# Kernel tuning notes

Measured on AMD Instinct MI355X. Metric: run time of the kernel, lower is better.

The kernel has to match this reference:

```python
import jax, jax.numpy as jnp
from jax import lax
import numpy as np

B, N, C = 16, 4096, 64
NPOINT, NSAMPLE, RADIUS = 1024, 32, 0.2


def farthest_point_sample(xyz, npoint):
    # xyz: (B, N, 3) -> (B, npoint) int32 indices
    b, n, _ = xyz.shape

    def body(carry, _):
        dists, farthest = carry  # (B,N), (B,)
        centroid = jnp.take_along_axis(xyz, farthest[:, None, None], axis=1)  # (B,1,3)
        d = jnp.sum((xyz - centroid) ** 2, axis=-1)  # (B,N)
        dists = jnp.minimum(dists, d)
        nxt = jnp.argmax(dists, axis=-1).astype(jnp.int32)
        return (dists, nxt), farthest

    init = (jnp.full((b, n), 1e10, xyz.dtype), jnp.zeros((b,), jnp.int32))
    _, idx = lax.scan(body, init, None, length=npoint)
    return idx.T  # (B, npoint)


def ball_query(radius, nsample, xyz, new_xyz):
    # xyz: (B,N,3), new_xyz: (B,S,3) -> (B,S,nsample) int32
    n = xyz.shape[1]
    # squared distances via ||a||^2 - 2ab + ||b||^2 to avoid (B,S,N,3) temp
    sqr = (jnp.sum(new_xyz ** 2, -1)[:, :, None]
           - 2.0 * jnp.einsum('bsc,bnc->bsn', new_xyz, xyz)
           + jnp.sum(xyz ** 2, -1)[:, None, :])  # (B,S,N)
    cand = jnp.broadcast_to(jnp.arange(n, dtype=jnp.int32), sqr.shape)
    cand = jnp.where(sqr > radius * radius, n, cand)  # out-of-ball -> sentinel N
    idx = jnp.sort(cand, axis=-1)[..., :nsample]  # first nsample in-ball indices
    first = idx[..., :1]
    return jnp.where(idx == n, first, idx)  # pad with first neighbor


def gather_points(pts, idx):
    # pts: (B,N,C), idx: (B,S,K) -> (B,S,K,C)
    return jax.vmap(lambda p, i: p[i])(pts, idx)


def setup_inputs() -> dict:
    key = jax.random.key(0)
    ks = jax.random.split(key, 8)
    c_in = C + 3  # use_xyz=True
    mlp = [64, 64, 128]
    inp = {
        'xyz': jax.random.uniform(ks[0], (B, N, 3), dtype=jnp.float32),
        'points': jax.random.normal(ks[1], (B, N, C), dtype=jnp.float32),
    }
    dims = [c_in] + mlp
    for i in range(3):
        fan_in = dims[i]
        inp[f'w{i}'] = jax.random.normal(ks[2 + i], (dims[i], dims[i + 1]), dtype=jnp.float32) / np.sqrt(fan_in)
        inp[f'b{i}'] = jnp.zeros((dims[i + 1],), dtype=jnp.float32)
    return inp


def reference(xyz, points, w0, b0, w1, b1, w2, b2):
    fps_idx = farthest_point_sample(xyz, NPOINT)  # (B,S)
    new_xyz = jnp.take_along_axis(xyz, fps_idx[:, :, None], axis=1)  # (B,S,3)
    idx = ball_query(RADIUS, NSAMPLE, xyz, new_xyz)  # (B,S,K)

    grouped_xyz = gather_points(xyz, idx) - new_xyz[:, :, None, :]  # (B,S,K,3) local coords
    grouped_pts = gather_points(points, idx)  # (B,S,K,C)
    new_points = jnp.concatenate([grouped_xyz, grouped_pts], axis=-1)  # (B,S,K,3+C)

    for w, b in ((w0, b0), (w1, b1), (w2, b2)):  # pointwise 1x1 Conv2d MLP, relu, no bn
        new_points = jax.nn.relu(jnp.einsum('bskc,cd->bskd', new_points, w) + b)

    new_points = jnp.max(new_points, axis=2)  # max-pool over nsample -> (B,S,128)
    return new_xyz, new_points
```

## Files before the change

### kernel.cpp

```cpp
#include <hip/hip_runtime.h>
#include <cstdint>

#define Bn 16
#define Nn 4096
#define Cn 64
#define NPOINT 1024
#define NSAMPLE 32

typedef float f32x2 __attribute__((ext_vector_type(2)));

__device__ __forceinline__ unsigned long long fps_wave_max(unsigned long long k) {
#define FPS_STEP(CTRL)                                                          \
  {                                                                             \
    unsigned int lo = (unsigned int)k, hi = (unsigned int)(k >> 32);            \
    unsigned int tlo =                                                          \
        (unsigned int)__builtin_amdgcn_update_dpp((int)lo, (int)lo, CTRL, 0xF, 0xF, false); \
    unsigned int thi =                                                          \
        (unsigned int)__builtin_amdgcn_update_dpp((int)hi, (int)hi, CTRL, 0xF, 0xF, false); \
    unsigned long long t = ((unsigned long long)thi << 32) | tlo;               \
    if (t > k) k = t;                                                           \
  }
  FPS_STEP(0x111)
  FPS_STEP(0x112)
  FPS_STEP(0x114)
  FPS_STEP(0x118)
  FPS_STEP(0x142)
  FPS_STEP(0x143)
#undef FPS_STEP
  return k;
}

__global__ __launch_bounds__(256) void fps_kernel(const float* __restrict__ xyz,
                                                  float* __restrict__ new_xyz) {
  const int b = blockIdx.x;
  const int t = threadIdx.x;
  const float* px = xyz + b * Nn * 3;

  __shared__ __align__(16) float4 sp[Nn];
  __shared__ __align__(16) float sc[NPOINT * 3];
  __shared__ __align__(16) unsigned long long rk[2][4];

  f32x2 X2[8], Y2[8], Z2[8], D2[8];
#pragma unroll
  for (int p = 0; p < 8; ++p) {
    int i0 = (2 * p) * 256 + t;
    int i1 = (2 * p + 1) * 256 + t;
    float x0 = px[i0 * 3 + 0], y0 = px[i0 * 3 + 1], z0 = px[i0 * 3 + 2];
    float x1 = px[i1 * 3 + 0], y1 = px[i1 * 3 + 1], z1 = px[i1 * 3 + 2];
    sp[i0] = make_float4(x0, y0, z0, 0.0f);
    sp[i1] = make_float4(x1, y1, z1, 0.0f);
    X2[p] = (f32x2){x0, x1};
    Y2[p] = (f32x2){y0, y1};
    Z2[p] = (f32x2){z0, z1};
    D2[p] = (f32x2){1e10f, 1e10f};
  }
  __syncthreads();

  int far = 0;

  for (int it = 0; it < NPOINT; ++it) {
    float4 c = sp[far];
    if (t == 0) {
      sc[it * 3 + 0] = c.x;
      sc[it * 3 + 1] = c.y;
      sc[it * 3 + 2] = c.z;
    }

    f32x2 cx2 = {c.x, c.x};
    f32x2 cy2 = {c.y, c.y};
    f32x2 cz2 = {c.z, c.z};

    float bd = -1.0f;
    int   bi = 0;
#pragma unroll
    for (int p = 0; p < 8; ++p) {
#pragma clang fp contract(off)
      f32x2 dx = X2[p] - cx2;
      f32x2 dy = Y2[p] - cy2;
      f32x2 dz = Z2[p] - cz2;
      f32x2 d2 = (dx * dx + dy * dy) + dz * dz;
      f32x2 nd = __builtin_elementwise_min(D2[p], d2);
      D2[p] = nd;
      float n0 = nd[0];
      if (n0 > bd) { bd = n0; bi = (2 * p) * 256 + t; }
      float n1 = nd[1];
      if (n1 > bd) { bd = n1; bi = (2 * p + 1) * 256 + t; }
    }

    unsigned long long k =
        ((unsigned long long)__float_as_uint(bd) << 32) |
        (unsigned int)(~(unsigned int)bi);
    k = fps_wave_max(k);

    const int buf = it & 1;
    if ((t & 63) == 63) rk[buf][t >> 6] = k;
    __syncthreads();

    unsigned long long f0 = rk[buf][0];
    unsigned long long f1 = rk[buf][1];
    unsigned long long f2 = rk[buf][2];
    unsigned long long f3 = rk[buf][3];
    if (f1 > f0) f0 = f1;
    if (f2 > f0) f0 = f2;
    if (f3 > f0) f0 = f3;
    far = (int)(~(unsigned int)f0);
  }

  float* out = new_xyz + b * NPOINT * 3;
  for (int i = t; i < NPOINT * 3; i += 256) out[i] = sc[i];
}

__global__ __launch_bounds__(256) void ballquery_kernel(const float* __restrict__ xyz,
                                                        const float* __restrict__ new_xyz,
                                                        int* __restrict__ bidx) {
  const int gw = (int)((blockIdx.x * 256 + threadIdx.x) >> 6);
  const int lane = threadIdx.x & 63;
  if (gw >= Bn * NPOINT) return;
  const int b = gw >> 10;
  const float* px = xyz + b * Nn * 3;
  const float R2 = 0.04f;

  float cx = new_xyz[gw * 3 + 0];
  float cy = new_xyz[gw * 3 + 1];
  float cz = new_xyz[gw * 3 + 2];
  float cs;
  {
#pragma clang fp contract(off)
    cs = (cx * cx + cy * cy) + cz * cz;
  }

  int* out = bidx + gw * NSAMPLE;
  int found = 0;
  int first = -1;

  for (int base = 0; base < Nn && found < NSAMPLE; base += 64) {
    int i = base + lane;
    float x = px[i * 3 + 0];
    float y = px[i * 3 + 1];
    float z = px[i * 3 + 2];
    float ps, sqr;
    float dot = fmaf(cx, x, 0.0f);
    dot = fmaf(cy, y, dot);
    dot = fmaf(cz, z, dot);
    {
#pragma clang fp contract(off)
      ps = (x * x + y * y) + z * z;
      sqr = (cs - 2.0f * dot) + ps;
    }
    bool pass = !(sqr > R2);
    unsigned long long m = __ballot(pass);
    if (first < 0 && m) first = base + (__ffsll(m) - 1);
    int rank = (int)__popcll(m & ((1ULL << lane) - 1ULL));
    int pos = found + rank;
    if (pass && pos < NSAMPLE) out[pos] = i;
    found += (int)__popcll(m);
  }

  int cnt = found < NSAMPLE ? found : NSAMPLE;
  for (int k = cnt + lane; k < NSAMPLE; k += 64) out[k] = first;
}

__global__ __launch_bounds__(64) void group_mlp_kernel(
    const float* __restrict__ xyz, const float* __restrict__ points,
    const float* __restrict__ w0, const float* __restrict__ b0,
    const float* __restrict__ w1, const float* __restrict__ b1,
    const float* __restrict__ w2, const float* __restrict__ b2,
    const float* __restrict__ new_xyz, const int* __restrict__ bidx,
    float* __restrict__ out_pts) {
  const int lane = threadIdx.x & 63;
  const int g = blockIdx.x;
  const int b = g >> 10;

  __shared__ __align__(16) float Xw[NSAMPLE][68];
  __shared__ __align__(16) float Hw[NSAMPLE][64];

  const int* bi = bidx + g * NSAMPLE;
  const float c0 = new_xyz[g * 3 + 0];
  const float c1 = new_xyz[g * 3 + 1];
  const float c2 = new_xyz[g * 3 + 2];

  for (int k = 0; k < NSAMPLE; ++k) {
    int id = bi[k];
    float v;
    if (lane < 3) {
      v = xyz[(b * Nn + id) * 3 + lane] - (lane == 0 ? c0 : (lane == 1 ? c1 : c2));
    } else {
      v = points[(b * Nn + id) * Cn + (lane - 3)];
    }
    Xw[k][lane] = v;
    if (lane < 3) Xw[k][64 + lane] = points[(b * Nn + id) * Cn + 61 + lane];
  }

  float acc[NSAMPLE];

  {
    float bb = b0[lane];
#pragma unroll
    for (int k = 0; k < NSAMPLE; ++k) acc[k] = bb;
    for (int c4 = 0; c4 < 16; ++c4) {
      float wa = w0[(c4 * 4 + 0) * 64 + lane];
      float wb = w0[(c4 * 4 + 1) * 64 + lane];
      float wc = w0[(c4 * 4 + 2) * 64 + lane];
      float wd = w0[(c4 * 4 + 3) * 64 + lane];
#pragma unroll
      for (int k = 0; k < NSAMPLE; ++k) {
        float4 xv = *(const float4*)&Xw[k][c4 * 4];
        acc[k] += xv.x * wa + xv.y * wb + xv.z * wc + xv.w * wd;
      }
    }
    float wt0 = w0[64 * 64 + lane];
    float wt1 = w0[65 * 64 + lane];
    float wt2 = w0[66 * 64 + lane];
#pragma unroll
    for (int k = 0; k < NSAMPLE; ++k)
      acc[k] += Xw[k][64] * wt0 + Xw[k][65] * wt1 + Xw[k][66] * wt2;
#pragma unroll
    for (int k = 0; k < NSAMPLE; ++k) Hw[k][lane] = fmaxf(acc[k], 0.0f);
  }

  {
    float bb = b1[lane];
#pragma unroll
    for (int k = 0; k < NSAMPLE; ++k) acc[k] = bb;
    for (int c4 = 0; c4 < 16; ++c4) {
      float wa = w1[(c4 * 4 + 0) * 64 + lane];
      float wb = w1[(c4 * 4 + 1) * 64 + lane];
      float wc = w1[(c4 * 4 + 2) * 64 + lane];
      float wd = w1[(c4 * 4 + 3) * 64 + lane];
#pragma unroll
      for (int k = 0; k < NSAMPLE; ++k) {
        float4 hv = *(const float4*)&Hw[k][c4 * 4];
        acc[k] += hv.x * wa + hv.y * wb + hv.z * wc + hv.w * wd;
      }
    }
#pragma unroll
    for (int k = 0; k < NSAMPLE; ++k) Xw[k][lane] = fmaxf(acc[k], 0.0f);
  }

  {
    float accB[NSAMPLE];
    float bbA = b2[lane];
    float bbB = b2[lane + 64];
#pragma unroll
    for (int k = 0; k < NSAMPLE; ++k) { acc[k] = bbA; accB[k] = bbB; }
    for (int c4 = 0; c4 < 16; ++c4) {
      float wa = w2[(c4 * 4 + 0) * 128 + lane];
      float wb = w2[(c4 * 4 + 1) * 128 + lane];
      float wc = w2[(c4 * 4 + 2) * 128 + lane];
      float wd = w2[(c4 * 4 + 3) * 128 + lane];
      float we = w2[(c4 * 4 + 0) * 128 + lane + 64];
      float wf = w2[(c4 * 4 + 1) * 128 + lane + 64];
      float wg = w2[(c4 * 4 + 2) * 128 + lane + 64];
      float wh = w2[(c4 * 4 + 3) * 128 + lane + 64];
#pragma unroll
      for (int k = 0; k < NSAMPLE; ++k) {
        float4 xv = *(const float4*)&Xw[k][c4 * 4];
        acc[k]  += xv.x * wa + xv.y * wb + xv.z * wc + xv.w * wd;
        accB[k] += xv.x * we + xv.y * wf + xv.z * wg + xv.w * wh;
      }
    }
    float mA = 0.0f, mB = 0.0f;
#pragma unroll
    for (int k = 0; k < NSAMPLE; ++k) {
      mA = fmaxf(mA, acc[k]);
      mB = fmaxf(mB, accB[k]);
    }
    float* outp = out_pts + g * 128;
    outp[lane] = mA;
    outp[lane + 64] = mB;
  }
}

extern "C" void kernel_launch(void* const* d_in, const int* in_sizes, int n_in,
                              void* d_out, int out_size, void* d_ws, size_t ws_size,
                              hipStream_t stream) {
  const float* xyz    = (const float*)d_in[0];
  const float* points = (const float*)d_in[1];
  const float* w0     = (const float*)d_in[2];
  const float* b0     = (const float*)d_in[3];
  const float* w1     = (const float*)d_in[4];
  const float* b1     = (const float*)d_in[5];
  const float* w2     = (const float*)d_in[6];
  const float* b2     = (const float*)d_in[7];

  float* new_xyz = (float*)d_out;
  float* new_pts = (float*)d_out + Bn * NPOINT * 3;
  int*   bidx    = (int*)d_ws;

  fps_kernel<<<Bn, 256, 0, stream>>>(xyz, new_xyz);
  ballquery_kernel<<<(Bn * NPOINT) / 4, 256, 0, stream>>>(xyz, new_xyz, bidx);
  group_mlp_kernel<<<Bn * NPOINT, 64, 0, stream>>>(xyz, points, w0, b0, w1, b1,
                                                   w2, b2, new_xyz, bidx, new_pts);
}
```

Baseline: 1.198 ms.

## Widen FPS block to 512 threads and remap MLP to one sample per lane

FPS now runs 512 threads per batch, so each thread holds half as many points and the per-iteration distance loop is shorter, at the cost of a wider cross-wave reduction. The grouped MLP kernel is restructured so that each lane owns one neighbor sample and keeps 64 output-channel accumulators in registers. Weights are read as uniform broadcast loads, and two groups are processed per 64-lane block. The max-pool becomes a shuffle-xor reduction across 32 lanes. This removes the per-sample LDS float4 reads, but it raises register pressure and adds 5 shuffle rounds over 64 values per pass.

```diff
diff --git a/kernel.cpp b/kernel.cpp
--- a/kernel.cpp
+++ b/kernel.cpp
@@ -6,6 +6,11 @@
 #define Cn 64
 #define NPOINT 1024
 #define NSAMPLE 32
+
+#define FPS_T 512
+#define FPS_W (FPS_T / 64)
+#define FPS_P (Nn / FPS_T)
+#define FPS_PAIRS (FPS_P / 2)
 
 typedef float f32x2 __attribute__((ext_vector_type(2)));
 
@@ -30,21 +35,21 @@
   return k;
 }
 
-__global__ __launch_bounds__(256) void fps_kernel(const float* __restrict__ xyz,
-                                                  float* __restrict__ new_xyz) {
+__global__ __launch_bounds__(FPS_T) void fps_kernel(const float* __restrict__ xyz,
+                                                    float* __restrict__ new_xyz) {
   const int b = blockIdx.x;
   const int t = threadIdx.x;
   const float* px = xyz + b * Nn * 3;
 
   __shared__ __align__(16) float4 sp[Nn];
   __shared__ __align__(16) float sc[NPOINT * 3];
-  __shared__ __align__(16) unsigned long long rk[2][4];
-
-  f32x2 X2[8], Y2[8], Z2[8], D2[8];
-#pragma unroll
-  for (int p = 0; p < 8; ++p) {
-    int i0 = (2 * p) * 256 + t;
-    int i1 = (2 * p + 1) * 256 + t;
+  __shared__ __align__(16) unsigned long long rk[2][FPS_W];
+
+  f32x2 X2[FPS_PAIRS], Y2[FPS_PAIRS], Z2[FPS_PAIRS], D2[FPS_PAIRS];
+#pragma unroll
+  for (int p = 0; p < FPS_PAIRS; ++p) {
+    int i0 = (2 * p) * FPS_T + t;
+    int i1 = (2 * p + 1) * FPS_T + t;
     float x0 = px[i0 * 3 + 0], y0 = px[i0 * 3 + 1], z0 = px[i0 * 3 + 2];
     float x1 = px[i1 * 3 + 0], y1 = px[i1 * 3 + 1], z1 = px[i1 * 3 + 2];
     sp[i0] = make_float4(x0, y0, z0, 0.0f);
@@ -73,7 +78,7 @@
     float bd = -1.0f;
     int   bi = 0;
 #pragma unroll
-    for (int p = 0; p < 8; ++p) {
+    for (int p = 0; p < FPS_PAIRS; ++p) {
 #pragma clang fp contract(off)
       f32x2 dx = X2[p] - cx2;
       f32x2 dy = Y2[p] - cy2;
@@ -82,9 +87,9 @@
       f32x2 nd = __builtin_elementwise_min(D2[p], d2);
       D2[p] = nd;
       float n0 = nd[0];
-      if (n0 > bd) { bd = n0; bi = (2 * p) * 256 + t; }
+      if (n0 > bd) { bd = n0; bi = (2 * p) * FPS_T + t; }
       float n1 = nd[1];
-      if (n1 > bd) { bd = n1; bi = (2 * p + 1) * 256 + t; }
+      if (n1 > bd) { bd = n1; bi = (2 * p + 1) * FPS_T + t; }
     }
 
     unsigned long long k =
@@ -97,17 +102,16 @@
     __syncthreads();
 
     unsigned long long f0 = rk[buf][0];
-    unsigned long long f1 = rk[buf][1];
-    unsigned long long f2 = rk[buf][2];
-    unsigned long long f3 = rk[buf][3];
-    if (f1 > f0) f0 = f1;
-    if (f2 > f0) f0 = f2;
-    if (f3 > f0) f0 = f3;
+#pragma unroll
+    for (int w = 1; w < FPS_W; ++w) {
+      unsigned long long fw = rk[buf][w];
+      if (fw > f0) f0 = fw;
+    }
     far = (int)(~(unsigned int)f0);
   }
 
   float* out = new_xyz + b * NPOINT * 3;
-  for (int i = t; i < NPOINT * 3; i += 256) out[i] = sc[i];
+  for (int i = t; i < NPOINT * 3; i += FPS_T) out[i] = sc[i];
 }
 
 __global__ __launch_bounds__(256) void ballquery_kernel(const float* __restrict__ xyz,
@@ -167,107 +171,86 @@
     const float* __restrict__ w2, const float* __restrict__ b2,
     const float* __restrict__ new_xyz, const int* __restrict__ bidx,
     float* __restrict__ out_pts) {
-  const int lane = threadIdx.x & 63;
-  const int g = blockIdx.x;
+  const int lane = threadIdx.x;
+  const int k = lane & 31;
+  const int g = blockIdx.x * 2 + (lane >> 5);
   const int b = g >> 10;
 
-  __shared__ __align__(16) float Xw[NSAMPLE][68];
-  __shared__ __align__(16) float Hw[NSAMPLE][64];
-
-  const int* bi = bidx + g * NSAMPLE;
-  const float c0 = new_xyz[g * 3 + 0];
-  const float c1 = new_xyz[g * 3 + 1];
-  const float c2 = new_xyz[g * 3 + 2];
-
-  for (int k = 0; k < NSAMPLE; ++k) {
-    int id = bi[k];
-    float v;
-    if (lane < 3) {
-      v = xyz[(b * Nn + id) * 3 + lane] - (lane == 0 ? c0 : (lane == 1 ? c1 : c2));
-    } else {
-      v = points[(b * Nn + id) * Cn + (lane - 3)];
-    }
-    Xw[k][lane] = v;
-    if (lane < 3) Xw[k][64 + lane] = points[(b * Nn + id) * Cn + 61 + lane];
-  }
-
-  float acc[NSAMPLE];
+  __shared__ float Xs[68][64];
+
+  const int id = bidx[g * NSAMPLE + k];
 
   {
-    float bb = b0[lane];
-#pragma unroll
-    for (int k = 0; k < NSAMPLE; ++k) acc[k] = bb;
-    for (int c4 = 0; c4 < 16; ++c4) {
-      float wa = w0[(c4 * 4 + 0) * 64 + lane];
-      float wb = w0[(c4 * 4 + 1) * 64 + lane];
-      float wc = w0[(c4 * 4 + 2) * 64 + lane];
-      float wd = w0[(c4 * 4 + 3) * 64 + lane];
-#pragma unroll
-      for (int k = 0; k < NSAMPLE; ++k) {
-        float4 xv = *(const float4*)&Xw[k][c4 * 4];
-        acc[k] += xv.x * wa + xv.y * wb + xv.z * wc + xv.w * wd;
-      }
-    }
-    float wt0 = w0[64 * 64 + lane];
-    float wt1 = w0[65 * 64 + lane];
-    float wt2 = w0[66 * 64 + lane];
-#pragma unroll
-    for (int k = 0; k < NSAMPLE; ++k)
-      acc[k] += Xw[k][64] * wt0 + Xw[k][65] * wt1 + Xw[k][66] * wt2;
-#pragma unroll
-    for (int k = 0; k < NSAMPLE; ++k) Hw[k][lane] = fmaxf(acc[k], 0.0f);
-  }
-
+    const float* p3 = xyz + (b * Nn + id) * 3;
+    Xs[0][lane] = p3[0] - new_xyz[g * 3 + 0];
+    Xs[1][lane] = p3[1] - new_xyz[g * 3 + 1];
+    Xs[2][lane] = p3[2] - new_xyz[g * 3 + 2];
+  }
   {
-    float bb = b1[lane];
-#pragma unroll
-    for (int k = 0; k < NSAMPLE; ++k) acc[k] = bb;
-    for (int c4 = 0; c4 < 16; ++c4) {
-      float wa = w1[(c4 * 4 + 0) * 64 + lane];
-      float wb = w1[(c4 * 4 + 1) * 64 + lane];
-      float wc = w1[(c4 * 4 + 2) * 64 + lane];
-      float wd = w1[(c4 * 4 + 3) * 64 + lane];
-#pragma unroll
-      for (int k = 0; k < NSAMPLE; ++k) {
-        float4 hv = *(const float4*)&Hw[k][c4 * 4];
-        acc[k] += hv.x * wa + hv.y * wb + hv.z * wc + hv.w * wd;
-      }
-    }
-#pragma unroll
-    for (int k = 0; k < NSAMPLE; ++k) Xw[k][lane] = fmaxf(acc[k], 0.0f);
-  }
-
-  {
-    float accB[NSAMPLE];
-    float bbA = b2[lane];
-    float bbB = b2[lane + 64];
-#pragma unroll
-    for (int k = 0; k < NSAMPLE; ++k) { acc[k] = bbA; accB[k] = bbB; }
-    for (int c4 = 0; c4 < 16; ++c4) {
-      float wa = w2[(c4 * 4 + 0) * 128 + lane];
-      float wb = w2[(c4 * 4 + 1) * 128 + lane];
-      float wc = w2[(c4 * 4 + 2) * 128 + lane];
-      float wd = w2[(c4 * 4 + 3) * 128 + lane];
-      float we = w2[(c4 * 4 + 0) * 128 + lane + 64];
-      float wf = w2[(c4 * 4 + 1) * 128 + lane + 64];
-      float wg = w2[(c4 * 4 + 2) * 128 + lane + 64];
-      float wh = w2[(c4 * 4 + 3) * 128 + lane + 64];
-#pragma unroll
-      for (int k = 0; k < NSAMPLE; ++k) {
-        float4 xv = *(const float4*)&Xw[k][c4 * 4];
-        acc[k]  += xv.x * wa + xv.y * wb + xv.z * wc + xv.w * wd;
-        accB[k] += xv.x * we + xv.y * wf + xv.z * wg + xv.w * wh;
-      }
-    }
-    float mA = 0.0f, mB = 0.0f;
-#pragma unroll
-    for (int k = 0; k < NSAMPLE; ++k) {
-      mA = fmaxf(mA, acc[k]);
-      mB = fmaxf(mB, accB[k]);
-    }
-    float* outp = out_pts + g * 128;
-    outp[lane] = mA;
-    outp[lane + 64] = mB;
+    const float* prow = points + (size_t)(b * Nn + id) * Cn;
+#pragma unroll
+    for (int q = 0; q < 16; ++q) {
+      float4 v = *(const float4*)(prow + q * 4);
+      Xs[3 + q * 4 + 0][lane] = v.x;
+      Xs[3 + q * 4 + 1][lane] = v.y;
+      Xs[3 + q * 4 + 2][lane] = v.z;
+      Xs[3 + q * 4 + 3][lane] = v.w;
+    }
+  }
+
+  float A[64];
+
+#pragma unroll
+  for (int d = 0; d < 64; ++d) A[d] = 0.0f;
+  for (int c = 0; c < 67; ++c) {
+    float xc = Xs[c][lane];
+    const float* wr = w0 + c * 64;
+#pragma unroll
+    for (int d = 0; d < 64; ++d) A[d] = fmaf(xc, wr[d], A[d]);
+  }
+#pragma unroll
+  for (int d = 0; d < 64; ++d) A[d] = fmaxf(A[d] + b0[d], 0.0f);
+#pragma unroll
+  for (int d = 0; d < 64; ++d) Xs[d][lane] = A[d];
+
+#pragma unroll
+  for (int d = 0; d < 64; ++d) A[d] = 0.0f;
+  for (int c = 0; c < 64; ++c) {
+    float xc = Xs[c][lane];
+    const float* wr = w1 + c * 64;
+#pragma unroll
+    for (int d = 0; d < 64; ++d) A[d] = fmaf(xc, wr[d], A[d]);
+  }
+#pragma unroll
+  for (int d = 0; d < 64; ++d) A[d] = fmaxf(A[d] + b1[d], 0.0f);
+#pragma unroll
+  for (int d = 0; d < 64; ++d) Xs[d][lane] = A[d];
+
+  float* outp = out_pts + (size_t)g * 128;
+#pragma unroll 1
+  for (int pass = 0; pass < 2; ++pass) {
+#pragma unroll
+    for (int d = 0; d < 64; ++d) A[d] = 0.0f;
+    for (int c = 0; c < 64; ++c) {
+      float xc = Xs[c][lane];
+      const float* wr = w2 + c * 128 + pass * 64;
+#pragma unroll
+      for (int d = 0; d < 64; ++d) A[d] = fmaf(xc, wr[d], A[d]);
+    }
+#pragma unroll
+    for (int d = 0; d < 64; ++d) A[d] = fmaxf(A[d] + b2[pass * 64 + d], 0.0f);
+
+#pragma unroll 1
+    for (int off = 1; off < 32; off <<= 1) {
+#pragma unroll
+      for (int d = 0; d < 64; ++d) A[d] = fmaxf(A[d], __shfl_xor(A[d], off, 64));
+    }
+    if (k == 0) {
+#pragma unroll
+      for (int q = 0; q < 16; ++q)
+        *(float4*)(outp + pass * 64 + q * 4) =
+            make_float4(A[q * 4 + 0], A[q * 4 + 1], A[q * 4 + 2], A[q * 4 + 3]);
+    }
   }
 }
 
@@ -287,8 +270,9 @@
   float* new_pts = (float*)d_out + Bn * NPOINT * 3;
   int*   bidx    = (int*)d_ws;
 
-  fps_kernel<<<Bn, 256, 0, stream>>>(xyz, new_xyz);
+  fps_kernel<<<Bn, FPS_T, 0, stream>>>(xyz, new_xyz);
   ballquery_kernel<<<(Bn * NPOINT) / 4, 256, 0, stream>>>(xyz, new_xyz, bidx);
-  group_mlp_kernel<<<Bn * NPOINT, 64, 0, stream>>>(xyz, points, w0, b0, w1, b1,
-                                                   w2, b2, new_xyz, bidx, new_pts);
-}
+  group_mlp_kernel<<<(Bn * NPOINT) / 2, 64, 0, stream>>>(xyz, points, w0, b0,
+                                                         w1, b1, w2, b2,
+                                                         new_xyz, bidx, new_pts);
+}
```

Result: faster. 1.124 ms (-6.2%).
